# Kernel optimization log

Hardware: AMD Instinct MI355X
Metric: run time of the kernel (lower is better)

The kernel has to match this reference:

```python
import jax, jax.numpy as jnp
import numpy as np

H = 8          # num_heads
NUM_SEEDS = 4  # num_seeds (T = T0 + NUM_SEEDS in training/non_trivial)
NEG_INF = float('-inf')


def setup_inputs() -> dict:
    key = jax.random.key(0)
    ks = jax.random.split(key, 9)
    B, T, L, C = 4, 16, 64, 512
    T0 = T - NUM_SEEDS
    x = jax.random.normal(ks[0], (B, T0 * L, C), dtype=jnp.float32)
    x_ctx = jax.random.normal(ks[1], (B, T, L, C), dtype=jnp.float32)
    dx_ctx = jax.random.normal(ks[2], (B, T, L, C), dtype=jnp.float32)
    ctx_mask = jax.random.randint(ks[3], (B, T), 0, 2).astype(jnp.bool_)
    s = 1.0 / np.sqrt(C)
    qkv_w = jax.random.normal(ks[4], (3 * C, C), dtype=jnp.float32) * s
    k_w = jax.random.normal(ks[5], (C, C), dtype=jnp.float32) * s
    v_w = jax.random.normal(ks[6], (C, C), dtype=jnp.float32) * s
    proj_w = jax.random.normal(ks[7], (C, C), dtype=jnp.float32) * s
    proj_b = jax.random.normal(ks[8], (C,), dtype=jnp.float32) * 0.01
    return {"x": x, "x_ctx": x_ctx, "dx_ctx": dx_ctx, "ctx_mask": ctx_mask,
            "qkv_w": qkv_w, "k_w": k_w, "v_w": v_w, "proj_w": proj_w,
            "proj_b": proj_b}


def reference(x, x_ctx, dx_ctx, ctx_mask, qkv_w, k_w, v_w, proj_w, proj_b):
    B, T, L, C = x_ctx.shape
    T0 = x.shape[1] // L
    hd = C // H
    scale = hd ** (-0.5)

    # qkv for the current (self) tokens: [3, B, H, T0*L, hd]
    qkv = (x @ qkv_w.T).reshape(B, T0 * L, 3, H, hd).transpose(2, 0, 3, 1, 4)
    q, k, v = qkv[0], qkv[1], qkv[2]

    # context keys/values: [B, H, T*L, hd]
    k_ctx = (dx_ctx.reshape(B, T * L, C) @ k_w.T).reshape(B, T * L, H, hd).transpose(0, 2, 1, 3)
    v_ctx = (x_ctx.reshape(B, T * L, C) @ v_w.T).reshape(B, T * L, H, hd).transpose(0, 2, 1, 3)

    # cross-context scores: [B, H, T0*L, T, L]
    attn = (jnp.einsum('bhqd,bhkd->bhqk', q, k_ctx) * scale).reshape(B, H, T0 * L, T, L)

    # context mask: drop whole context frames where ctx_mask is False
    attn = jnp.where(ctx_mask[:, None, None, :, None], attn, NEG_INF)

    # non-trivial temporal mask (training): query frame i can't attend to
    # context frame i + num_seeds
    nt = (jnp.arange(T0)[:, None] + NUM_SEEDS) == jnp.arange(T)[None, :]  # [T0, T]
    attn6 = attn.reshape(B, H, T0, L, T, L)
    attn6 = jnp.where(nt[None, None, :, None, :, None], NEG_INF, attn6)
    attn = attn6.reshape(B, H, T0 * L, T, L)

    # per-frame self attention scores: [B, H, T0, L, L] -> [B, H, T0*L, 1, L]
    q6 = q.reshape(B, H, T0, L, hd)
    k6 = k.reshape(B, H, T0, L, hd)
    self_attn = (jnp.einsum('bhtqd,bhtkd->bhtqk', q6, k6) * scale).reshape(B, H, T0 * L, 1, L)

    # joint softmax over (T+1)*L keys
    attn = jnp.concatenate([attn, self_attn], axis=-2).reshape(B, H, T0 * L, (T + 1) * L)
    attn = jax.nn.softmax(attn, axis=-1)

    # split back: cross part @ v_ctx, self part @ v (per frame)
    out = jnp.einsum('bhqk,bhkd->bhqd', attn[:, :, :, :-L], v_ctx)
    a_self = attn[:, :, :, -L:].reshape(B, H, T0, L, L)
    v6 = v.reshape(B, H, T0, L, hd)
    out = out + jnp.einsum('bhtqk,bhtkd->bhtqd', a_self, v6).reshape(B, H, T0 * L, hd)

    out = out.transpose(0, 2, 1, 3).reshape(B, T0 * L, C)
    return out @ proj_w.T + proj_b
```

## Files before the change

### kernel.cpp

```cpp
#include <hip/hip_runtime.h>
#include <hip/hip_bf16.h>

typedef __attribute__((ext_vector_type(8))) short bf16x8;
typedef __attribute__((ext_vector_type(4))) float f32x4;

#define BB 4
#define TT 16
#define NT0 12
#define LL 64
#define CC 512
#define HH 8
#define HD 64
#define NQ (NT0*LL)
#define NCTX (TT*LL)

#define GPTR(x) ((__attribute__((address_space(1))) void*)(x))
#define SPTR(x) ((__attribute__((address_space(3))) void*)(x))
#define VMCNT(n) (((n) & 15) | (7u << 4) | (0xFu << 8))

__device__ __forceinline__ float bf2f(ushort u) {
  union { unsigned int i; float f; } x; x.i = ((unsigned int)u) << 16; return x.f;
}
__device__ __forceinline__ ushort f2bf(float f) {
  union { float f; unsigned int i; } x; x.f = f;
  unsigned int r = x.i + 0x7fffu + ((x.i >> 16) & 1u);
  return (ushort)(r >> 16);
}

__global__ __launch_bounds__(256) void cvt_all(const float* __restrict__ w0,
                                               const float* __restrict__ w1,
                                               const float* __restrict__ w2,
                                               const float* __restrict__ w3,
                                               const float* __restrict__ x,
                                               const float* __restrict__ xc,
                                               const float* __restrict__ dxc,
                                               ushort* __restrict__ dst) {
  long i = (long)blockIdx.x * 256 + threadIdx.x;
  const float* src; long off;
  if (i < 196608)       { src = w0;  off = 0; }
  else if (i < 262144)  { src = w1;  off = 196608; }
  else if (i < 327680)  { src = w2;  off = 262144; }
  else if (i < 393216)  { src = w3;  off = 327680; }
  else if (i < 786432)  { src = x;   off = 393216; }
  else if (i < 1310720) { src = xc;  off = 786432; }
  else                  { src = dxc; off = 1310720; }
  f32x4 v = *(const f32x4*)(src + (i - off) * 4);
  ushort4 o = { f2bf(v[0]), f2bf(v[1]), f2bf(v[2]), f2bf(v[3]) };
  *(ushort4*)(dst + i * 4) = o;
}

template<int MT>
__device__ __forceinline__ void gemm_mac(const ushort* __restrict__ A,
                                         const ushort* __restrict__ W,
                                         int mt, int nt, ushort* lds,
                                         f32x4* acc) {
  constexpr int ACH = MT * 4;
  constexpr int ASZ = MT * 32;
  constexpr int BUF = ASZ + 4096;
  constexpr int L   = (MT == 128) ? 4 : 3;

  int t = threadIdx.x;
  int pa0 = t, pa1 = t + 256;
  int ra0 = pa0 >> 2, ra1 = pa1 >> 2;
  int ca0 = (pa0 & 3) ^ ((ra0 >> 1) & 3);
  int ca1 = (pa1 & 3) ^ ((ra1 >> 1) & 3);
  int pw0 = t, pw1 = t + 256;
  const ushort* ga0 = A + (size_t)(mt * MT + ra0) * 512 + ca0 * 8;
  const ushort* ga1 = A + (size_t)(mt * MT + ra1) * 512 + ca1 * 8;
  const ushort* gw0 = W + (size_t)(nt * 128 + ra0) * 512 + ca0 * 8;
  const ushort* gw1 = W + (size_t)(nt * 128 + ra1) * 512 + ca1 * 8;

  int lane = t & 63, l15 = lane & 15, kg = lane >> 4;
  int wv = t >> 6;
  int mh = (wv >> 1) * (MT / 2), nh = (wv & 1) * 64;
  int swz = kg ^ ((l15 >> 1) & 3);
  int faoff = (mh + l15) * 32 + swz * 8;
  int fwoff = (nh + l15) * 32 + swz * 8;

  auto stage = [&](int ks, int bb) {
    int ko = ks * 32;
    __builtin_amdgcn_global_load_lds(GPTR(ga0 + ko), SPTR(lds + bb + pa0 * 8), 16, 0, 0);
    if (MT == 128)
      __builtin_amdgcn_global_load_lds(GPTR(ga1 + ko), SPTR(lds + bb + pa1 * 8), 16, 0, 0);
    __builtin_amdgcn_global_load_lds(GPTR(gw0 + ko), SPTR(lds + bb + ASZ + pw0 * 8), 16, 0, 0);
    __builtin_amdgcn_global_load_lds(GPTR(gw1 + ko), SPTR(lds + bb + ASZ + pw1 * 8), 16, 0, 0);
  };

  stage(0, 0);
  stage(1, BUF);

#pragma unroll
  for (int ks = 0; ks < 16; ++ks) {
    int cur = (ks % 3) * BUF;
    if (ks < 14) {
      stage(ks + 2, ((ks + 2) % 3) * BUF);
      __builtin_amdgcn_s_waitcnt(VMCNT(2 * L));
    } else if (ks == 14) {
      __builtin_amdgcn_s_waitcnt(VMCNT(L));
    } else {
      __builtin_amdgcn_s_waitcnt(VMCNT(0));
    }
    asm volatile("" ::: "memory");
    __builtin_amdgcn_s_barrier();
    asm volatile("" ::: "memory");

    const ushort* fa = lds + cur + faoff;
    const ushort* fw = lds + cur + ASZ + fwoff;
    bf16x8 af[MT / 32], wf[4];
#pragma unroll
    for (int i = 0; i < MT / 32; ++i) af[i] = *(const bf16x8*)(fa + i * 512);
#pragma unroll
    for (int i = 0; i < 4; ++i) wf[i] = *(const bf16x8*)(fw + i * 512);
#pragma unroll
    for (int mi = 0; mi < MT / 32; ++mi)
#pragma unroll
      for (int ni = 0; ni < 4; ++ni)
        acc[mi * 4 + ni] =
            __builtin_amdgcn_mfma_f32_16x16x32_bf16(af[mi], wf[ni], acc[mi * 4 + ni], 0, 0, 0);

    asm volatile("" ::: "memory");
    __builtin_amdgcn_s_barrier();
    asm volatile("" ::: "memory");
  }
}

template<int MT, int OUTMODE>
__device__ __forceinline__ void gemm_body(const ushort* __restrict__ A,
                                          const ushort* __restrict__ W,
                                          ushort* __restrict__ C,
                                          ushort* __restrict__ CT,
                                          float* __restrict__ Cf,
                                          const float* __restrict__ bias,
                                          int mt, int nt, int N, long TM,
                                          ushort* lds) {
  f32x4 acc[(MT / 32) * 4];
#pragma unroll
  for (int i = 0; i < (MT / 32) * 4; ++i) acc[i] = (f32x4){0, 0, 0, 0};
  gemm_mac<MT>(A, W, mt, nt, lds, acc);

  int lane = threadIdx.x & 63, l15 = lane & 15, kg = lane >> 4;
  int wv = threadIdx.x >> 6;
  int Rw = mt * MT + (wv >> 1) * (MT / 2);
  int Cw = nt * 128 + (wv & 1) * 64;
#pragma unroll
  for (int mi = 0; mi < MT / 32; ++mi) {
    int row = Rw + mi * 16 + kg * 4;
#pragma unroll
    for (int ni = 0; ni < 4; ++ni) {
      f32x4 v = acc[mi * 4 + ni];
      int col = Cw + ni * 16 + l15;
      if (OUTMODE == 0) {
#pragma unroll
        for (int r = 0; r < 4; ++r) C[(size_t)(row + r) * N + col] = f2bf(v[r]);
      } else if (OUTMODE == 1) {
        ushort4 o = { f2bf(v[0]), f2bf(v[1]), f2bf(v[2]), f2bf(v[3]) };
        *(ushort4*)(CT + (long)col * TM + row) = o;
      } else {
        float bv = bias[col];
#pragma unroll
        for (int r = 0; r < 4; ++r) Cf[(size_t)(row + r) * N + col] = v[r] + bv;
      }
    }
  }
}

__global__ __launch_bounds__(256) void gemm3(const ushort* __restrict__ xb,
                                             const ushort* __restrict__ dxb,
                                             const ushort* __restrict__ xcb,
                                             const ushort* __restrict__ qkvwb,
                                             const ushort* __restrict__ kwb,
                                             const ushort* __restrict__ vwb,
                                             ushort* __restrict__ qkv,
                                             ushort* __restrict__ vselfT,
                                             ushort* __restrict__ kctx,
                                             ushort* __restrict__ vctxT) {
  __shared__ ushort lds[24576];
  int blk = blockIdx.x;
  if (blk < 288) {
    int mt = blk % 24, nt = blk / 24;
    if (nt < 8)
      gemm_body<128, 0>(xb, qkvwb, qkv, nullptr, nullptr, nullptr, mt, nt, 1536, 0, lds);
    else
      gemm_body<128, 1>(xb, qkvwb, nullptr, vselfT - (size_t)1024 * 3072, nullptr, nullptr,
                        mt, nt, 1536, 3072, lds);
  } else if (blk < 416) {
    int r = blk - 288;
    gemm_body<128, 0>(dxb, kwb, kctx, nullptr, nullptr, nullptr, r % 32, r / 32, 512, 0, lds);
  } else {
    int r = blk - 416;
    gemm_body<128, 1>(xcb, vwb, nullptr, vctxT, nullptr, nullptr, r % 32, r / 32, 512, 4096, lds);
  }
}

__global__ __launch_bounds__(256) void gemm_proj(const ushort* __restrict__ aout,
                                                 const ushort* __restrict__ pwb,
                                                 const float* __restrict__ bias,
                                                 float* __restrict__ out) {
  __shared__ ushort lds[18432];
  int blk = blockIdx.x;
  gemm_body<64, 2>(aout, pwb, nullptr, nullptr, out, bias, blk % 48, blk / 48, 512, 0, lds);
}

__device__ __forceinline__ void attn_tile(const ushort* __restrict__ kbase, int kstr,
                                          const ushort* __restrict__ vtb, int vtN,
                                          bf16x8 q0, bf16x8 q1,
                                          int l15, int kg,
                                          ushort* __restrict__ myPt,
                                          f32x4* acc, float& Lacc) {
  f32x4 s[4];
#pragma unroll
  for (int st = 0; st < 4; ++st) {
    const ushort* kp = kbase + (size_t)(st * 16 + l15) * kstr + kg * 8;
    bf16x8 k0 = *(const bf16x8*)kp;
    bf16x8 k1 = *(const bf16x8*)(kp + 32);
    f32x4 z = {0, 0, 0, 0};
    z = __builtin_amdgcn_mfma_f32_16x16x32_bf16(k0, q0, z, 0, 0, 0);
    z = __builtin_amdgcn_mfma_f32_16x16x32_bf16(k1, q1, z, 0, 0, 0);
    s[st] = z;
  }
#pragma unroll
  for (int st = 0; st < 4; ++st) {
    float p0 = __builtin_exp2f(fmaf(s[st][0], 0.18033688f, -23.0831206f));
    float p1 = __builtin_exp2f(fmaf(s[st][1], 0.18033688f, -23.0831206f));
    float p2 = __builtin_exp2f(fmaf(s[st][2], 0.18033688f, -23.0831206f));
    float p3 = __builtin_exp2f(fmaf(s[st][3], 0.18033688f, -23.0831206f));
    Lacc += (p0 + p1) + (p2 + p3);
    ushort4 pk = { f2bf(p0), f2bf(p1), f2bf(p2), f2bf(p3) };
    *(ushort4*)(myPt + l15 * 72 + st * 16 + kg * 4) = pk;
  }
#pragma unroll
  for (int kc = 0; kc < 2; ++kc) {
    bf16x8 pb = *(const bf16x8*)(myPt + l15 * 72 + kc * 32 + kg * 8);
#pragma unroll
    for (int d = 0; d < 4; ++d) {
      const ushort* vp = vtb + (size_t)(d * 16 + l15) * vtN + kc * 32 + kg * 8;
      bf16x8 vf = *(const bf16x8*)vp;
      acc[d] = __builtin_amdgcn_mfma_f32_16x16x32_bf16(vf, pb, acc[d], 0, 0, 0);
    }
  }
}

__global__ __launch_bounds__(512) void flash_attn(const ushort* __restrict__ qkv,
                                                  const ushort* __restrict__ kctx,
                                                  const ushort* __restrict__ vctxT,
                                                  const ushort* __restrict__ vselfT,
                                                  const int* __restrict__ ctx_mask,
                                                  ushort* __restrict__ aout) {
  __shared__ ushort sm[18432];
  int blk = blockIdx.x;
  int qh = blk & 1;
  int rest = blk >> 1;
  int t0 = rest % NT0;
  int h  = (rest / NT0) % HH;
  int b  = rest / (NT0 * HH);
  int tid = threadIdx.x, wv = tid >> 6, lane = tid & 63;
  int qg = wv & 1, ks = wv >> 1;
  int l15 = lane & 15, kg = lane >> 4;

  int qrow = b * NQ + t0 * LL + qh * 32 + qg * 16 + l15;
  const ushort* qp = qkv + (size_t)qrow * 1536 + h * HD + kg * 8;
  bf16x8 q0 = *(const bf16x8*)qp;
  bf16x8 q1 = *(const bf16x8*)(qp + 32);

  f32x4 acc[4] = {{0,0,0,0},{0,0,0,0},{0,0,0,0},{0,0,0,0}};
  float Lacc = 0.f;
  ushort* Pt0 = sm + wv * 2304;

  int kts[4]; int nkt = 0;
#pragma unroll
  for (int ki = 0; ki < 4; ++ki) {
    int kt = ks * 4 + ki;
    if (ctx_mask[b * TT + kt] != 0 && kt != t0 + 4) kts[nkt++] = kt;
  }

  const ushort* vctxb = vctxT + (size_t)h * HD * (BB * NCTX) + b * NCTX;
  int buf = 0;
  for (int ki = 0; ki < nkt; ++ki) {
    int kt = kts[ki];
    attn_tile(kctx + (size_t)(b * NCTX + kt * LL) * CC + h * HD, CC,
              vctxb + kt * LL, BB * NCTX,
              q0, q1, l15, kg, Pt0 + buf * 1152, acc, Lacc);
    buf ^= 1;
  }
  if (ks == 0) {
    attn_tile(qkv + (size_t)(b * NQ + t0 * LL) * 1536 + CC + h * HD, 1536,
              vselfT + (size_t)h * HD * (BB * NQ) + b * NQ + t0 * LL, BB * NQ,
              q0, q1, l15, kg, Pt0 + buf * 1152, acc, Lacc);
  }

  float Lr = Lacc;
  Lr += __shfl_xor(Lr, 16, 64);
  Lr += __shfl_xor(Lr, 32, 64);

  __syncthreads();
  float* fsm = (float*)sm;
  if (ks) {
    float* reg = fsm + (size_t)(qg * 3 + ks - 1) * 1088;
#pragma unroll
    for (int d = 0; d < 4; ++d) *(f32x4*)(reg + lane * 16 + d * 4) = acc[d];
    reg[1024 + lane] = Lr;
  }
  __syncthreads();
  if (!ks) {
    float Ls = Lr;
    f32x4 o[4];
#pragma unroll
    for (int d = 0; d < 4; ++d) o[d] = acc[d];
#pragma unroll
    for (int j = 0; j < 3; ++j) {
      const float* reg = fsm + (size_t)(qg * 3 + j) * 1088;
      Ls += reg[1024 + lane];
#pragma unroll
      for (int d = 0; d < 4; ++d)
        o[d] += *(const f32x4*)(reg + lane * 16 + d * 4);
    }
    float inv = 1.f / Ls;
    int orow = b * NQ + t0 * LL + qh * 32 + qg * 16 + l15;
#pragma unroll
    for (int d = 0; d < 4; ++d) {
      ushort4 ov = { f2bf(o[d][0] * inv), f2bf(o[d][1] * inv),
                     f2bf(o[d][2] * inv), f2bf(o[d][3] * inv) };
      *(ushort4*)(aout + (size_t)orow * CC + h * HD + d * 16 + kg * 4) = ov;
    }
  }
}

extern "C" void kernel_launch(void* const* d_in, const int* in_sizes, int n_in,
                              void* d_out, int out_size, void* d_ws, size_t ws_size,
                              hipStream_t stream) {
  const float* x        = (const float*)d_in[0];
  const float* x_ctx    = (const float*)d_in[1];
  const float* dx_ctx   = (const float*)d_in[2];
  const int*   ctx_mask = (const int*)d_in[3];
  const float* qkv_w    = (const float*)d_in[4];
  const float* k_w      = (const float*)d_in[5];
  const float* v_w      = (const float*)d_in[6];
  const float* proj_w   = (const float*)d_in[7];
  const float* proj_b   = (const float*)d_in[8];
  float* out = (float*)d_out;

  ushort* ws = (ushort*)d_ws;
  ushort* qkvwb  = ws;
  ushort* kwb    = ws + 786432;
  ushort* vwb    = ws + 1048576;
  ushort* pwb    = ws + 1310720;
  ushort* xb     = ws + 1572864;
  ushort* xcb    = ws + 3145728;
  ushort* dxb    = ws + 5242880;
  ushort* qkv    = ws + 7340032;
  ushort* kctx   = ws + 12058624;
  ushort* vctxT  = ws + 14155776;
  ushort* vselfT = ws + 16252928;
  ushort* aout   = ws + 17825792;

  cvt_all<<<7168, 256, 0, stream>>>(qkv_w, k_w, v_w, proj_w, x, x_ctx, dx_ctx, ws);
  gemm3<<<544, 256, 0, stream>>>(xb, dxb, xcb, qkvwb, kwb, vwb,
                                 qkv, vselfT, kctx, vctxT);
  flash_attn<<<768, 512, 0, stream>>>(qkv, kctx, vctxT, vselfT, ctx_mask, aout);
  gemm_proj<<<192, 256, 0, stream>>>(aout, pwb, proj_b, out);
}
```

Measured before the change: 144.1 us.

## Process 32 query rows per wave in flash attention to reuse K/V fragments

Each wave now computes two 16-row query fragments against the same K and V loads, doubling register-level reuse of K/V fragments. Blocks now cover all 64 queries of a frame, halving the grid to 384 blocks, and the launch bounds add an occupancy hint. The per-wave P buffers and the cross-wave reduction buffers are resized to match. The cost is more registers per wave and fewer blocks, which could reduce parallelism across the GPU's compute units.

```diff
diff --git a/kernel.cpp b/kernel.cpp
--- a/kernel.cpp
+++ b/kernel.cpp
@@ -54,7 +54,6 @@
                                          const ushort* __restrict__ W,
                                          int mt, int nt, ushort* lds,
                                          f32x4* acc) {
-  constexpr int ACH = MT * 4;
   constexpr int ASZ = MT * 32;
   constexpr int BUF = ASZ + 4096;
   constexpr int L   = (MT == 128) ? 4 : 3;
@@ -64,7 +63,6 @@
   int ra0 = pa0 >> 2, ra1 = pa1 >> 2;
   int ca0 = (pa0 & 3) ^ ((ra0 >> 1) & 3);
   int ca1 = (pa1 & 3) ^ ((ra1 >> 1) & 3);
-  int pw0 = t, pw1 = t + 256;
   const ushort* ga0 = A + (size_t)(mt * MT + ra0) * 512 + ca0 * 8;
   const ushort* ga1 = A + (size_t)(mt * MT + ra1) * 512 + ca1 * 8;
   const ushort* gw0 = W + (size_t)(nt * 128 + ra0) * 512 + ca0 * 8;
@@ -82,8 +80,8 @@
     __builtin_amdgcn_global_load_lds(GPTR(ga0 + ko), SPTR(lds + bb + pa0 * 8), 16, 0, 0);
     if (MT == 128)
       __builtin_amdgcn_global_load_lds(GPTR(ga1 + ko), SPTR(lds + bb + pa1 * 8), 16, 0, 0);
-    __builtin_amdgcn_global_load_lds(GPTR(gw0 + ko), SPTR(lds + bb + ASZ + pw0 * 8), 16, 0, 0);
-    __builtin_amdgcn_global_load_lds(GPTR(gw1 + ko), SPTR(lds + bb + ASZ + pw1 * 8), 16, 0, 0);
+    __builtin_amdgcn_global_load_lds(GPTR(gw0 + ko), SPTR(lds + bb + ASZ + pa0 * 8), 16, 0, 0);
+    __builtin_amdgcn_global_load_lds(GPTR(gw1 + ko), SPTR(lds + bb + ASZ + pa1 * 8), 16, 0, 0);
   };
 
   stage(0, 0);
@@ -201,70 +199,84 @@
   gemm_body<64, 2>(aout, pwb, nullptr, nullptr, out, bias, blk % 48, blk / 48, 512, 0, lds);
 }
 
-__device__ __forceinline__ void attn_tile(const ushort* __restrict__ kbase, int kstr,
-                                          const ushort* __restrict__ vtb, int vtN,
-                                          bf16x8 q0, bf16x8 q1,
-                                          int l15, int kg,
-                                          ushort* __restrict__ myPt,
-                                          f32x4* acc, float& Lacc) {
-  f32x4 s[4];
+__device__ __forceinline__ void attn_tile32(const ushort* __restrict__ kbase, int kstr,
+                                            const ushort* __restrict__ vtb, int vtN,
+                                            bf16x8 qa0, bf16x8 qa1,
+                                            bf16x8 qb0, bf16x8 qb1,
+                                            int l15, int kg,
+                                            ushort* __restrict__ Pt,
+                                            f32x4 (*acc)[4], float* Lacc) {
+  f32x4 s[2][4];
 #pragma unroll
   for (int st = 0; st < 4; ++st) {
     const ushort* kp = kbase + (size_t)(st * 16 + l15) * kstr + kg * 8;
     bf16x8 k0 = *(const bf16x8*)kp;
     bf16x8 k1 = *(const bf16x8*)(kp + 32);
-    f32x4 z = {0, 0, 0, 0};
-    z = __builtin_amdgcn_mfma_f32_16x16x32_bf16(k0, q0, z, 0, 0, 0);
-    z = __builtin_amdgcn_mfma_f32_16x16x32_bf16(k1, q1, z, 0, 0, 0);
-    s[st] = z;
-  }
-#pragma unroll
-  for (int st = 0; st < 4; ++st) {
-    float p0 = __builtin_exp2f(fmaf(s[st][0], 0.18033688f, -23.0831206f));
-    float p1 = __builtin_exp2f(fmaf(s[st][1], 0.18033688f, -23.0831206f));
-    float p2 = __builtin_exp2f(fmaf(s[st][2], 0.18033688f, -23.0831206f));
-    float p3 = __builtin_exp2f(fmaf(s[st][3], 0.18033688f, -23.0831206f));
-    Lacc += (p0 + p1) + (p2 + p3);
-    ushort4 pk = { f2bf(p0), f2bf(p1), f2bf(p2), f2bf(p3) };
-    *(ushort4*)(myPt + l15 * 72 + st * 16 + kg * 4) = pk;
+    f32x4 z0 = {0, 0, 0, 0}, z1 = {0, 0, 0, 0};
+    z0 = __builtin_amdgcn_mfma_f32_16x16x32_bf16(k0, qa0, z0, 0, 0, 0);
+    z0 = __builtin_amdgcn_mfma_f32_16x16x32_bf16(k1, qa1, z0, 0, 0, 0);
+    z1 = __builtin_amdgcn_mfma_f32_16x16x32_bf16(k0, qb0, z1, 0, 0, 0);
+    z1 = __builtin_amdgcn_mfma_f32_16x16x32_bf16(k1, qb1, z1, 0, 0, 0);
+    s[0][st] = z0;
+    s[1][st] = z1;
+  }
+#pragma unroll
+  for (int qf = 0; qf < 2; ++qf) {
+#pragma unroll
+    for (int st = 0; st < 4; ++st) {
+      float p0 = __builtin_exp2f(fmaf(s[qf][st][0], 0.18033688f, -23.0831206f));
+      float p1 = __builtin_exp2f(fmaf(s[qf][st][1], 0.18033688f, -23.0831206f));
+      float p2 = __builtin_exp2f(fmaf(s[qf][st][2], 0.18033688f, -23.0831206f));
+      float p3 = __builtin_exp2f(fmaf(s[qf][st][3], 0.18033688f, -23.0831206f));
+      Lacc[qf] += (p0 + p1) + (p2 + p3);
+      ushort4 pk = { f2bf(p0), f2bf(p1), f2bf(p2), f2bf(p3) };
+      *(ushort4*)(Pt + qf * 1152 + l15 * 72 + st * 16 + kg * 4) = pk;
+    }
   }
 #pragma unroll
   for (int kc = 0; kc < 2; ++kc) {
-    bf16x8 pb = *(const bf16x8*)(myPt + l15 * 72 + kc * 32 + kg * 8);
+    bf16x8 pb0 = *(const bf16x8*)(Pt + l15 * 72 + kc * 32 + kg * 8);
+    bf16x8 pb1 = *(const bf16x8*)(Pt + 1152 + l15 * 72 + kc * 32 + kg * 8);
 #pragma unroll
     for (int d = 0; d < 4; ++d) {
       const ushort* vp = vtb + (size_t)(d * 16 + l15) * vtN + kc * 32 + kg * 8;
       bf16x8 vf = *(const bf16x8*)vp;
-      acc[d] = __builtin_amdgcn_mfma_f32_16x16x32_bf16(vf, pb, acc[d], 0, 0, 0);
-    }
-  }
-}
-
-__global__ __launch_bounds__(512) void flash_attn(const ushort* __restrict__ qkv,
-                                                  const ushort* __restrict__ kctx,
-                                                  const ushort* __restrict__ vctxT,
-                                                  const ushort* __restrict__ vselfT,
-                                                  const int* __restrict__ ctx_mask,
-                                                  ushort* __restrict__ aout) {
-  __shared__ ushort sm[18432];
+      acc[0][d] = __builtin_amdgcn_mfma_f32_16x16x32_bf16(vf, pb0, acc[0][d], 0, 0, 0);
+      acc[1][d] = __builtin_amdgcn_mfma_f32_16x16x32_bf16(vf, pb1, acc[1][d], 0, 0, 0);
+    }
+  }
+}
+
+__global__ __launch_bounds__(512, 4) void flash_attn(const ushort* __restrict__ qkv,
+                                                     const ushort* __restrict__ kctx,
+                                                     const ushort* __restrict__ vctxT,
+                                                     const ushort* __restrict__ vselfT,
+                                                     const int* __restrict__ ctx_mask,
+                                                     ushort* __restrict__ aout) {
+  __shared__ float smem[13056];
   int blk = blockIdx.x;
-  int qh = blk & 1;
-  int rest = blk >> 1;
-  int t0 = rest % NT0;
-  int h  = (rest / NT0) % HH;
-  int b  = rest / (NT0 * HH);
+  int t0 = blk % NT0;
+  int h  = (blk / NT0) % HH;
+  int b  = blk / (NT0 * HH);
   int tid = threadIdx.x, wv = tid >> 6, lane = tid & 63;
-  int qg = wv & 1, ks = wv >> 1;
+  int qg = wv >> 2, ks = wv & 3;
   int l15 = lane & 15, kg = lane >> 4;
 
-  int qrow = b * NQ + t0 * LL + qh * 32 + qg * 16 + l15;
-  const ushort* qp = qkv + (size_t)qrow * 1536 + h * HD + kg * 8;
-  bf16x8 q0 = *(const bf16x8*)qp;
-  bf16x8 q1 = *(const bf16x8*)(qp + 32);
-
-  f32x4 acc[4] = {{0,0,0,0},{0,0,0,0},{0,0,0,0},{0,0,0,0}};
-  float Lacc = 0.f;
-  ushort* Pt0 = sm + wv * 2304;
+  int qbase = b * NQ + t0 * LL + qg * 32;
+  const ushort* qp0 = qkv + (size_t)(qbase + l15) * 1536 + h * HD + kg * 8;
+  const ushort* qp1 = qkv + (size_t)(qbase + 16 + l15) * 1536 + h * HD + kg * 8;
+  bf16x8 qa0 = *(const bf16x8*)qp0;
+  bf16x8 qa1 = *(const bf16x8*)(qp0 + 32);
+  bf16x8 qb0 = *(const bf16x8*)qp1;
+  bf16x8 qb1 = *(const bf16x8*)(qp1 + 32);
+
+  f32x4 acc[2][4];
+#pragma unroll
+  for (int qf = 0; qf < 2; ++qf)
+#pragma unroll
+    for (int d = 0; d < 4; ++d) acc[qf][d] = (f32x4){0, 0, 0, 0};
+  float Lacc[2] = {0.f, 0.f};
+  ushort* Pt = (ushort*)smem + wv * 2304;
 
   int kts[4]; int nkt = 0;
 #pragma unroll
@@ -274,53 +286,62 @@
   }
 
   const ushort* vctxb = vctxT + (size_t)h * HD * (BB * NCTX) + b * NCTX;
-  int buf = 0;
   for (int ki = 0; ki < nkt; ++ki) {
     int kt = kts[ki];
-    attn_tile(kctx + (size_t)(b * NCTX + kt * LL) * CC + h * HD, CC,
-              vctxb + kt * LL, BB * NCTX,
-              q0, q1, l15, kg, Pt0 + buf * 1152, acc, Lacc);
-    buf ^= 1;
+    attn_tile32(kctx + (size_t)(b * NCTX + kt * LL) * CC + h * HD, CC,
+                vctxb + kt * LL, BB * NCTX,
+                qa0, qa1, qb0, qb1, l15, kg, Pt, acc, Lacc);
   }
   if (ks == 0) {
-    attn_tile(qkv + (size_t)(b * NQ + t0 * LL) * 1536 + CC + h * HD, 1536,
-              vselfT + (size_t)h * HD * (BB * NQ) + b * NQ + t0 * LL, BB * NQ,
-              q0, q1, l15, kg, Pt0 + buf * 1152, acc, Lacc);
-  }
-
-  float Lr = Lacc;
-  Lr += __shfl_xor(Lr, 16, 64);
-  Lr += __shfl_xor(Lr, 32, 64);
+    attn_tile32(qkv + (size_t)(b * NQ + t0 * LL) * 1536 + CC + h * HD, 1536,
+                vselfT + (size_t)h * HD * (BB * NQ) + b * NQ + t0 * LL, BB * NQ,
+                qa0, qa1, qb0, qb1, l15, kg, Pt, acc, Lacc);
+  }
+
+  float L0 = Lacc[0], L1 = Lacc[1];
+  L0 += __shfl_xor(L0, 16, 64); L0 += __shfl_xor(L0, 32, 64);
+  L1 += __shfl_xor(L1, 16, 64); L1 += __shfl_xor(L1, 32, 64);
 
   __syncthreads();
-  float* fsm = (float*)sm;
   if (ks) {
-    float* reg = fsm + (size_t)(qg * 3 + ks - 1) * 1088;
-#pragma unroll
-    for (int d = 0; d < 4; ++d) *(f32x4*)(reg + lane * 16 + d * 4) = acc[d];
-    reg[1024 + lane] = Lr;
+    float* reg = smem + (size_t)(qg * 3 + ks - 1) * 2176;
+#pragma unroll
+    for (int qf = 0; qf < 2; ++qf)
+#pragma unroll
+      for (int d = 0; d < 4; ++d)
+        *(f32x4*)(reg + (qf * 64 + lane) * 16 + d * 4) = acc[qf][d];
+    reg[2048 + lane * 2]     = L0;
+    reg[2048 + lane * 2 + 1] = L1;
   }
   __syncthreads();
   if (!ks) {
-    float Ls = Lr;
-    f32x4 o[4];
-#pragma unroll
-    for (int d = 0; d < 4; ++d) o[d] = acc[d];
+    float Ls[2] = {L0, L1};
+    f32x4 o[2][4];
+#pragma unroll
+    for (int qf = 0; qf < 2; ++qf)
+#pragma unroll
+      for (int d = 0; d < 4; ++d) o[qf][d] = acc[qf][d];
 #pragma unroll
     for (int j = 0; j < 3; ++j) {
-      const float* reg = fsm + (size_t)(qg * 3 + j) * 1088;
-      Ls += reg[1024 + lane];
-#pragma unroll
-      for (int d = 0; d < 4; ++d)
-        o[d] += *(const f32x4*)(reg + lane * 16 + d * 4);
-    }
-    float inv = 1.f / Ls;
-    int orow = b * NQ + t0 * LL + qh * 32 + qg * 16 + l15;
-#pragma unroll
-    for (int d = 0; d < 4; ++d) {
-      ushort4 ov = { f2bf(o[d][0] * inv), f2bf(o[d][1] * inv),
-                     f2bf(o[d][2] * inv), f2bf(o[d][3] * inv) };
-      *(ushort4*)(aout + (size_t)orow * CC + h * HD + d * 16 + kg * 4) = ov;
+      const float* reg = smem + (size_t)(qg * 3 + j) * 2176;
+      Ls[0] += reg[2048 + lane * 2];
+      Ls[1] += reg[2048 + lane * 2 + 1];
+#pragma unroll
+      for (int qf = 0; qf < 2; ++qf)
+#pragma unroll
+        for (int d = 0; d < 4; ++d)
+          o[qf][d] += *(const f32x4*)(reg + (qf * 64 + lane) * 16 + d * 4);
+    }
+#pragma unroll
+    for (int qf = 0; qf < 2; ++qf) {
+      float inv = 1.f / Ls[qf];
+      int orow = qbase + qf * 16 + l15;
+#pragma unroll
+      for (int d = 0; d < 4; ++d) {
+        ushort4 ov = { f2bf(o[qf][d][0] * inv), f2bf(o[qf][d][1] * inv),
+                       f2bf(o[qf][d][2] * inv), f2bf(o[qf][d][3] * inv) };
+        *(ushort4*)(aout + (size_t)orow * CC + h * HD + d * 16 + kg * 4) = ov;
+      }
     }
   }
 }
@@ -356,6 +377,6 @@
   cvt_all<<<7168, 256, 0, stream>>>(qkv_w, k_w, v_w, proj_w, x, x_ctx, dx_ctx, ws);
   gemm3<<<544, 256, 0, stream>>>(xb, dxb, xcb, qkvwb, kwb, vwb,
                                  qkv, vselfT, kctx, vctxT);
-  flash_attn<<<768, 512, 0, stream>>>(qkv, kctx, vctxT, vselfT, ctx_mask, aout);
+  flash_attn<<<384, 512, 0, stream>>>(qkv, kctx, vctxT, vselfT, ctx_mask, aout);
   gemm_proj<<<192, 256, 0, stream>>>(aout, pwb, proj_b, out);
 }
```

Measured after the change: 139.7 us. 3.1% less time.
